# Performance work log

Measured on AMD Instinct MI355X. Metric: run time of the kernel, lower is better.

Reference implementation:

```python
import jax, jax.numpy as jnp
import numpy as np

B, S, H, NH = 4, 1024, 1024, 16
HD = H // NH
I = 4096
EPS = 1e-12
BASE = 10000.0


def setup_inputs() -> dict:
    key = jax.random.key(0)
    ks = jax.random.split(key, 6)
    sc = 0.02
    return {
        "x": jax.random.normal(ks[0], (B, S, H), jnp.float32),
        "ln1_w": jnp.ones((H,), jnp.float32),
        "ln1_b": jnp.zeros((H,), jnp.float32),
        "qkv_w": jax.random.normal(ks[1], (3 * H, H), jnp.float32) * sc,
        "qkv_b": jnp.zeros((3 * H,), jnp.float32),
        "out_w": jax.random.normal(ks[2], (H, H), jnp.float32) * sc,
        "out_b": jnp.zeros((H,), jnp.float32),
        "ln2_w": jnp.ones((H,), jnp.float32),
        "ln2_b": jnp.zeros((H,), jnp.float32),
        "i2h_w": jax.random.normal(ks[3], (2 * I, H), jnp.float32) * sc,
        "i2h_b": jnp.zeros((2 * I,), jnp.float32),
        "h2o_w": jax.random.normal(ks[4], (H, I), jnp.float32) * sc,
        "h2o_b": jnp.zeros((H,), jnp.float32),
    }


def _layer_norm(x, w, b, eps=EPS):
    mu = jnp.mean(x, axis=-1, keepdims=True)
    var = jnp.mean(jnp.square(x - mu), axis=-1, keepdims=True)
    return (x - mu) * jax.lax.rsqrt(var + eps) * w + b


def _rope_cos_sin(seq_len, dim, base):
    # inv_freq = base ** linspace(0, -1 + 2/dim, dim//2), repeated twice
    half = jnp.power(base, jnp.linspace(0.0, -1.0 + 2.0 / dim, dim // 2, dtype=jnp.float32))
    inv_freq = jnp.concatenate([half, half])  # [dim]
    t = jnp.arange(seq_len, dtype=jnp.float32)
    freqs = t[:, None] * inv_freq[None, :]  # [seq, dim]
    return jnp.cos(freqs), jnp.sin(freqs)


def _rotate(x, cos, sin):
    # x: [B, NH, S, HD]; cos/sin: [S, HD]
    xl, xr = jnp.split(x, 2, axis=-1)
    x_rot = jnp.concatenate([-xr, xl], axis=-1)
    return x * cos + x_rot * sin


def _forward(x, ln1_w, ln1_b, qkv_w, qkv_b, out_w, out_b,
             ln2_w, ln2_b, i2h_w, i2h_b, h2o_w, h2o_b):
    b, s, h = x.shape
    # --- LeanSelfAttention (pre-LN, rotary, causal, residual) ---
    h_ln = _layer_norm(x, ln1_w, ln1_b)
    qkv = h_ln @ qkv_w.T + qkv_b  # [b, s, 3h]
    q, k, v = jnp.split(qkv, 3, axis=-1)
    to_heads = lambda t: t.reshape(b, s, NH, HD).transpose(0, 2, 1, 3)  # [b,nh,s,hd]
    q, k, v = to_heads(q), to_heads(k), to_heads(v)
    cos, sin = _rope_cos_sin(s, HD, BASE)
    q, k = _rotate(q, cos, sin), _rotate(k, cos, sin)
    scores = jnp.einsum("bhqd,bhkd->bhqk", q, k) / np.sqrt(HD).astype(np.float32)
    causal = jnp.tril(jnp.ones((s, s), dtype=bool))
    scores = jnp.where(causal, scores, jnp.float32(-10000.0))
    probs = jax.nn.softmax(scores, axis=-1)
    attn = jnp.einsum("bhqk,bhkd->bhqd", probs, v)
    attn = attn.transpose(0, 2, 1, 3).reshape(b, s, h)
    attn_out = attn @ out_w.T + out_b + x  # residual
    # --- LeanFFN (pre-LN, gated gelu, residual) ---
    ffn_ln = _layer_norm(attn_out, ln2_w, ln2_b)
    pre = ffn_ln @ i2h_w.T + i2h_b  # [b, s, 2I]
    gate, lin = jnp.split(pre, 2, axis=-1)
    hid = jax.nn.gelu(gate, approximate=False) * lin
    return hid @ h2o_w.T + h2o_b + attn_out


def reference(x, ln1_w, ln1_b, qkv_w, qkv_b, out_w, out_b,
              ln2_w, ln2_b, i2h_w, i2h_b, h2o_w, h2o_b):
    return _forward(x, ln1_w, ln1_b, qkv_w, qkv_b, out_w, out_b,
                    ln2_w, ln2_b, i2h_w, i2h_b, h2o_w, h2o_b)
```

## Files before the change

### kernel.cpp

```cpp
#include <hip/hip_runtime.h>
#include <cstdint>
#include <cstddef>

typedef __bf16 bf16;
typedef __bf16 bf16x4 __attribute__((ext_vector_type(4)));
typedef __bf16 bf16x8 __attribute__((ext_vector_type(8)));
typedef float  f32x4  __attribute__((ext_vector_type(4)));

#define GLD16(gptr, lptr)                                                      \
  __builtin_amdgcn_global_load_lds(                                            \
      (__attribute__((address_space(1))) unsigned int*)(gptr),                 \
      (__attribute__((address_space(3))) unsigned int*)(lptr), 16, 0, 0)

__global__ __launch_bounds__(256)
void convert_kernel(const float* __restrict__ src, bf16* __restrict__ dst, int n8)
{
    const int j = blockIdx.x * 256 + threadIdx.x;
    if (j >= n8) return;
    const float* s = src + (size_t)j * 8;
    bf16x8 o;
#pragma unroll
    for (int e = 0; e < 8; ++e) o[e] = (bf16)s[e];
    ((bf16x8*)dst)[j] = o;
}

template<class InT>
__global__ __launch_bounds__(256)
void ln_kernel(const InT* __restrict__ x, const float* __restrict__ w,
               const float* __restrict__ b, bf16* __restrict__ out)
{
    __shared__ float red[8];
    const int row = blockIdx.x;
    const int tid = threadIdx.x;
    const InT* xr = x + (size_t)row * 1024;
    float xf[4], s = 0.f, ss = 0.f;
#pragma unroll
    for (int j = 0; j < 4; ++j) {
        xf[j] = (float)xr[tid * 4 + j];
        s += xf[j]; ss += xf[j] * xf[j];
    }
#pragma unroll
    for (int off = 32; off > 0; off >>= 1) { s += __shfl_xor(s, off); ss += __shfl_xor(ss, off); }
    if ((tid & 63) == 0) { red[(tid >> 6) * 2] = s; red[(tid >> 6) * 2 + 1] = ss; }
    __syncthreads();
    s  = red[0] + red[2] + red[4] + red[6];
    ss = red[1] + red[3] + red[5] + red[7];
    const float mu   = s * (1.f / 1024.f);
    const float var  = ss * (1.f / 1024.f) - mu * mu;
    const float rstd = rsqrtf(var + 1e-12f);
    bf16x4 ov;
#pragma unroll
    for (int j = 0; j < 4; ++j)
        ov[j] = (bf16)((xf[j] - mu) * rstd * w[tid * 4 + j] + b[tid * 4 + j]);
    *(bf16x4*)(out + (size_t)row * 1024 + tid * 4) = ov;
}

template<int RES_MODE, bool OUT_F32>
__global__ __launch_bounds__(256)
void gemm_bt(const bf16* __restrict__ A, const bf16* __restrict__ W,
             const float* __restrict__ bias, const void* __restrict__ res,
             void* __restrict__ Cv, int M, int N, int K)
{
    __shared__ alignas(16) bf16 As[128][32];
    __shared__ alignas(16) bf16 Bs[128][32];
    const int tid  = threadIdx.x;
    const int lane = tid & 63, wid = tid >> 6;
    const int lr = lane & 15, lg = lane >> 4;
    const int kgrp = lg * 8;
    const int wm = (wid >> 1) * 64, wn = (wid & 1) * 64;
    const int row0 = blockIdx.x * 128, col0 = blockIdx.y * 128;

    f32x4 acc[4][4] = {};

    for (int k0 = 0; k0 < K; k0 += 32) {
#pragma unroll
        for (int i = 0; i < 2; ++i) {
            const int c = i * 256 + tid;
            const int r = c >> 2, k8 = (c & 3) * 8;
            GLD16(A + (size_t)(row0 + r) * K + k0 + k8,
                  (char*)&As[0][0] + (size_t)(i * 256 + wid * 64) * 16);
            GLD16(W + (size_t)(col0 + r) * K + k0 + k8,
                  (char*)&Bs[0][0] + (size_t)(i * 256 + wid * 64) * 16);
        }
        __syncthreads();
        bf16x8 af[4], bw[4];
#pragma unroll
        for (int mi = 0; mi < 4; ++mi) af[mi] = *(const bf16x8*)&As[wm + mi * 16 + lr][kgrp];
#pragma unroll
        for (int ni = 0; ni < 4; ++ni) bw[ni] = *(const bf16x8*)&Bs[wn + ni * 16 + lr][kgrp];
#pragma unroll
        for (int mi = 0; mi < 4; ++mi)
#pragma unroll
            for (int ni = 0; ni < 4; ++ni)
                acc[mi][ni] = __builtin_amdgcn_mfma_f32_16x16x32_bf16(
                    af[mi], bw[ni], acc[mi][ni], 0, 0, 0);
        __syncthreads();
    }

#pragma unroll
    for (int ni = 0; ni < 4; ++ni) {
        const int ccol = col0 + wn + ni * 16 + lr;
        const float bv = bias[ccol];
#pragma unroll
        for (int mi = 0; mi < 4; ++mi)
#pragma unroll
            for (int r = 0; r < 4; ++r) {
                const size_t crow = (size_t)(row0 + wm + mi * 16 + lg * 4 + r);
                float v = acc[mi][ni][r] + bv;
                if constexpr (RES_MODE == 1) v += ((const float*)res)[crow * N + ccol];
                if constexpr (RES_MODE == 2) v += (float)((const bf16*)res)[crow * N + ccol];
                if constexpr (OUT_F32) ((float*)Cv)[crow * N + ccol] = v;
                else                   ((bf16*)Cv)[crow * N + ccol] = (bf16)v;
            }
    }
}

__global__ __launch_bounds__(256)
void gemm_i2h_gelu(const bf16* __restrict__ A, const bf16* __restrict__ W,
                   const float* __restrict__ bias, bf16* __restrict__ hid)
{
    __shared__ alignas(16) bf16 As[128][32];
    __shared__ alignas(16) bf16 Bg[64][32];
    __shared__ alignas(16) bf16 Bl[64][32];
    const int tid  = threadIdx.x;
    const int lane = tid & 63, wid = tid >> 6;
    const int lr = lane & 15, lg = lane >> 4;
    const int kgrp = lg * 8;
    const int wm = (wid >> 1) * 64, wn = (wid & 1) * 32;
    const int row0 = blockIdx.x * 128, col0 = blockIdx.y * 64;
    const int K = 1024;

    f32x4 accg[4][2] = {}, accl[4][2] = {};

    for (int k0 = 0; k0 < K; k0 += 32) {
#pragma unroll
        for (int i = 0; i < 2; ++i) {
            const int c = i * 256 + tid;
            const int r = c >> 2, k8 = (c & 3) * 8;
            GLD16(A + (size_t)(row0 + r) * K + k0 + k8,
                  (char*)&As[0][0] + (size_t)(i * 256 + wid * 64) * 16);
        }
        {
            const int r = tid >> 2, k8 = (tid & 3) * 8;
            GLD16(W + (size_t)(col0 + r) * K + k0 + k8,
                  (char*)&Bg[0][0] + (size_t)(wid * 64) * 16);
            GLD16(W + (size_t)(4096 + col0 + r) * K + k0 + k8,
                  (char*)&Bl[0][0] + (size_t)(wid * 64) * 16);
        }
        __syncthreads();
        bf16x8 af[4], bg[2], bl[2];
#pragma unroll
        for (int mi = 0; mi < 4; ++mi) af[mi] = *(const bf16x8*)&As[wm + mi * 16 + lr][kgrp];
#pragma unroll
        for (int ni = 0; ni < 2; ++ni) {
            bg[ni] = *(const bf16x8*)&Bg[wn + ni * 16 + lr][kgrp];
            bl[ni] = *(const bf16x8*)&Bl[wn + ni * 16 + lr][kgrp];
        }
#pragma unroll
        for (int mi = 0; mi < 4; ++mi)
#pragma unroll
            for (int ni = 0; ni < 2; ++ni) {
                accg[mi][ni] = __builtin_amdgcn_mfma_f32_16x16x32_bf16(
                    af[mi], bg[ni], accg[mi][ni], 0, 0, 0);
                accl[mi][ni] = __builtin_amdgcn_mfma_f32_16x16x32_bf16(
                    af[mi], bl[ni], accl[mi][ni], 0, 0, 0);
            }
        __syncthreads();
    }

#pragma unroll
    for (int ni = 0; ni < 2; ++ni) {
        const int gc = col0 + wn + ni * 16 + lr;
        const float bg_ = bias[gc], bl_ = bias[4096 + gc];
#pragma unroll
        for (int mi = 0; mi < 4; ++mi)
#pragma unroll
            for (int r = 0; r < 4; ++r) {
                const size_t crow = (size_t)(row0 + wm + mi * 16 + lg * 4 + r);
                const float g = accg[mi][ni][r] + bg_;
                const float l = accl[mi][ni][r] + bl_;
                const float ge = 0.5f * g * (1.f + erff(g * 0.70710678118654752f));
                hid[crow * 4096 + gc] = (bf16)(ge * l);
            }
    }
}

__global__ __launch_bounds__(256)
void rope_kernel(const bf16* __restrict__ qkv, bf16* __restrict__ q_r,
                 bf16* __restrict__ k_r, bf16* __restrict__ v_r)
{
    const int g  = blockIdx.x * 256 + threadIdx.x;
    const int i  = g & 31;
    const int h  = (g >> 5) & 15;
    const int bs = g >> 9;
    const int s  = bs & 1023;
    const bf16* base = qkv + (size_t)bs * 3072;
    const float inv = __expf((float)i * (-9.210340371976184f / 32.f));
    const float ang = (float)s * inv;
    float sn, c;
    sincosf(ang, &sn, &c);
    const int qoff = h * 64 + i;
    const float ql = (float)base[qoff],        qh = (float)base[qoff + 32];
    const float kl = (float)base[1024 + qoff], kh = (float)base[1024 + qoff + 32];
    const size_t ob = ((size_t)((bs >> 10) * 16 + h) * 1024 + s) * 64;
    q_r[ob + i]      = (bf16)(ql * c - qh * sn);
    q_r[ob + i + 32] = (bf16)(qh * c + ql * sn);
    k_r[ob + i]      = (bf16)(kl * c - kh * sn);
    k_r[ob + i + 32] = (bf16)(kh * c + kl * sn);
    v_r[ob + i]      = base[2048 + qoff];
    v_r[ob + i + 32] = base[2048 + qoff + 32];
}

__global__ __launch_bounds__(256)
void attn_kernel(const bf16* __restrict__ q_r, const bf16* __restrict__ k_r,
                 const bf16* __restrict__ v_r, bf16* __restrict__ attn)
{
    __shared__ alignas(16) bf16 Ks[64][72];
    __shared__ alignas(16) bf16 Vt[64][72];
    __shared__ alignas(16) bf16 Ps[4][16][72];
    const int qt = blockIdx.x, bh = blockIdx.y;
    const int tid = threadIdx.x, lane = tid & 63, w = tid >> 6;
    const int lr = lane & 15, lg = lane >> 4;
    const int kgrp = lg * 8;
    const int qbase = qt * 64;

    const bf16* qrow = q_r + ((size_t)bh * 1024 + qbase + w * 16 + lr) * 64;
    const bf16x8 qf0 = *(const bf16x8*)(qrow + kgrp);
    const bf16x8 qf1 = *(const bf16x8*)(qrow + 32 + kgrp);

    f32x4 o[4] = {};
    float m_r[4], l_r[4];
#pragma unroll
    for (int r = 0; r < 4; ++r) { m_r[r] = -1e30f; l_r[r] = 0.f; }

    const int nchunk = qt + 1;
    for (int ic = 0; ic < nchunk; ++ic) {
        const int kb = ic * 64;
        __syncthreads();
#pragma unroll
        for (int i = 0; i < 2; ++i) {
            const int c = i * 256 + tid;
            const int row = c >> 3, e8 = (c & 7) * 8;
            *(bf16x8*)&Ks[row][e8] =
                *(const bf16x8*)(k_r + ((size_t)bh * 1024 + kb + row) * 64 + e8);
            const bf16x8 vv =
                *(const bf16x8*)(v_r + ((size_t)bh * 1024 + kb + row) * 64 + e8);
#pragma unroll
            for (int j = 0; j < 8; ++j) Vt[e8 + j][row] = vv[j];
        }
        __syncthreads();

        f32x4 sv[4] = {};
#pragma unroll
        for (int nb = 0; nb < 4; ++nb) {
            const bf16x8 kf0 = *(const bf16x8*)&Ks[nb * 16 + lr][kgrp];
            const bf16x8 kf1 = *(const bf16x8*)&Ks[nb * 16 + lr][32 + kgrp];
            sv[nb] = __builtin_amdgcn_mfma_f32_16x16x32_bf16(qf0, kf0, sv[nb], 0, 0, 0);
            sv[nb] = __builtin_amdgcn_mfma_f32_16x16x32_bf16(qf1, kf1, sv[nb], 0, 0, 0);
        }

        const bool diag = (kb == qbase);
        float pv[4][4];
#pragma unroll
        for (int r = 0; r < 4; ++r) {
            float s0[4];
#pragma unroll
            for (int nb = 0; nb < 4; ++nb) {
                float t = sv[nb][r] * 0.125f;
                if (diag && (nb * 16 + lr) > (w * 16 + lg * 4 + r)) t = -10000.f;
                s0[nb] = t;
            }
            float rm = fmaxf(fmaxf(s0[0], s0[1]), fmaxf(s0[2], s0[3]));
#pragma unroll
            for (int off = 1; off < 16; off <<= 1) rm = fmaxf(rm, __shfl_xor(rm, off));
            const float nm = fmaxf(m_r[r], rm);
            const float sc = __expf(m_r[r] - nm);
            float rs = 0.f;
#pragma unroll
            for (int nb = 0; nb < 4; ++nb) {
                const float p = __expf(s0[nb] - nm);
                pv[nb][r] = p; rs += p;
            }
#pragma unroll
            for (int off = 1; off < 16; off <<= 1) rs += __shfl_xor(rs, off);
            l_r[r] = l_r[r] * sc + rs;
            m_r[r] = nm;
#pragma unroll
            for (int nb = 0; nb < 4; ++nb) o[nb][r] *= sc;
        }

#pragma unroll
        for (int nb = 0; nb < 4; ++nb)
#pragma unroll
            for (int r = 0; r < 4; ++r)
                Ps[w][lg * 4 + r][nb * 16 + lr] = (bf16)pv[nb][r];
#pragma unroll
        for (int nb = 0; nb < 4; ++nb)
#pragma unroll
            for (int ks = 0; ks < 2; ++ks) {
                const bf16x8 pa = *(const bf16x8*)&Ps[w][lr][ks * 32 + kgrp];
                const bf16x8 vb = *(const bf16x8*)&Vt[nb * 16 + lr][ks * 32 + kgrp];
                o[nb] = __builtin_amdgcn_mfma_f32_16x16x32_bf16(pa, vb, o[nb], 0, 0, 0);
            }
    }

    const int b = bh >> 4, head = bh & 15;
#pragma unroll
    for (int nb = 0; nb < 4; ++nb)
#pragma unroll
        for (int r = 0; r < 4; ++r) {
            const size_t rw = (size_t)(b * 1024 + qbase + w * 16 + lg * 4 + r);
            attn[rw * 1024 + head * 64 + nb * 16 + lr] = (bf16)(o[nb][r] / l_r[r]);
        }
}

extern "C" void kernel_launch(void* const* d_in, const int* in_sizes, int n_in,
                              void* d_out, int out_size, void* d_ws, size_t ws_size,
                              hipStream_t stream)
{
    const float* x    = (const float*)d_in[0];
    const float* ln1w = (const float*)d_in[1];
    const float* ln1b = (const float*)d_in[2];
    const float* qkvw = (const float*)d_in[3];
    const float* qkvb = (const float*)d_in[4];
    const float* outw = (const float*)d_in[5];
    const float* outb = (const float*)d_in[6];
    const float* ln2w = (const float*)d_in[7];
    const float* ln2b = (const float*)d_in[8];
    const float* i2hw = (const float*)d_in[9];
    const float* i2hb = (const float*)d_in[10];
    const float* h2ow = (const float*)d_in[11];
    const float* h2ob = (const float*)d_in[12];

    char* ws = (char*)d_ws;
    const size_t MB = 1024 * 1024;

    bf16* h_ln    = (bf16*)(ws + 0);
    bf16* qkv     = (bf16*)(ws + 8 * MB);
    bf16* q_r     = (bf16*)(ws + 32 * MB);
    bf16* k_r     = (bf16*)(ws + 40 * MB);
    bf16* v_r     = (bf16*)(ws + 48 * MB);
    bf16* attn    = (bf16*)(ws + 56 * MB);
    bf16* attnout = (bf16*)(ws + 64 * MB);
    bf16* ffnln   = (bf16*)(ws + 72 * MB);
    bf16* hid     = (bf16*)(ws + 80 * MB);
    bf16* qkvw_c  = (bf16*)(ws + 112 * MB);
    bf16* outw_c  = (bf16*)(ws + 118 * MB);
    bf16* i2hw_c  = (bf16*)(ws + 120 * MB);
    bf16* h2ow_c  = (bf16*)(ws + 136 * MB);

    convert_kernel<<<1536, 256, 0, stream>>>(qkvw, qkvw_c, 3145728 / 8);
    convert_kernel<<< 512, 256, 0, stream>>>(outw, outw_c, 1048576 / 8);
    convert_kernel<<<4096, 256, 0, stream>>>(i2hw, i2hw_c, 8388608 / 8);
    convert_kernel<<<2048, 256, 0, stream>>>(h2ow, h2ow_c, 4194304 / 8);

    ln_kernel<float><<<4096, 256, 0, stream>>>(x, ln1w, ln1b, h_ln);
    gemm_bt<0, false><<<dim3(32, 24), 256, 0, stream>>>(
        h_ln, qkvw_c, qkvb, nullptr, qkv, 4096, 3072, 1024);
    rope_kernel<<<8192, 256, 0, stream>>>(qkv, q_r, k_r, v_r);
    attn_kernel<<<dim3(16, 64), 256, 0, stream>>>(q_r, k_r, v_r, attn);
    gemm_bt<1, false><<<dim3(32, 8), 256, 0, stream>>>(
        attn, outw_c, outb, x, attnout, 4096, 1024, 1024);
    ln_kernel<bf16><<<4096, 256, 0, stream>>>(attnout, ln2w, ln2b, ffnln);
    gemm_i2h_gelu<<<dim3(32, 64), 256, 0, stream>>>(ffnln, i2hw_c, i2hb, hid);
    gemm_bt<2, true><<<dim3(32, 8), 256, 0, stream>>>(
        hid, h2ow_c, h2ob, attnout, d_out, 4096, 1024, 4096);
}
```

Before: 484.7 us.

## Fuse RoPE into QKV GEMM epilogue and pipeline i2h GEMM with triple-buffered LDS

The standalone rope kernel is removed: the QKV projection writes rotated Q/K and head-major V directly from its GEMM epilogue, pairing columns i and i+32 inside each 64-column warp tile. This drops the intermediate qkv buffer round trip and one launch. Separately, the gated i2h GEMM is rewritten with 512-thread blocks, 256x128 tiles, triple-buffered async global-to-LDS loads with XOR swizzling, and setprio around the MFMA bursts, to raise data reuse and overlap loads with compute. Risks include higher register pressure and less occupancy in the larger kernel, and the epilogue recomputing sincos per element.

```diff
diff --git a/kernel.cpp b/kernel.cpp
--- a/kernel.cpp
+++ b/kernel.cpp
@@ -116,21 +116,21 @@
 }
 
 __global__ __launch_bounds__(256)
-void gemm_i2h_gelu(const bf16* __restrict__ A, const bf16* __restrict__ W,
-                   const float* __restrict__ bias, bf16* __restrict__ hid)
+void gemm_qkv_rope(const bf16* __restrict__ A, const bf16* __restrict__ W,
+                   const float* __restrict__ bias, bf16* __restrict__ q_r,
+                   bf16* __restrict__ k_r, bf16* __restrict__ v_r)
 {
     __shared__ alignas(16) bf16 As[128][32];
-    __shared__ alignas(16) bf16 Bg[64][32];
-    __shared__ alignas(16) bf16 Bl[64][32];
+    __shared__ alignas(16) bf16 Bs[128][32];
     const int tid  = threadIdx.x;
     const int lane = tid & 63, wid = tid >> 6;
     const int lr = lane & 15, lg = lane >> 4;
     const int kgrp = lg * 8;
-    const int wm = (wid >> 1) * 64, wn = (wid & 1) * 32;
-    const int row0 = blockIdx.x * 128, col0 = blockIdx.y * 64;
+    const int wm = (wid >> 1) * 64, wn = (wid & 1) * 64;
+    const int row0 = blockIdx.x * 128, col0 = blockIdx.y * 128;
     const int K = 1024;
 
-    f32x4 accg[4][2] = {}, accl[4][2] = {};
+    f32x4 acc[4][4] = {};
 
     for (int k0 = 0; k0 < K; k0 += 32) {
 #pragma unroll
@@ -139,76 +139,162 @@
             const int r = c >> 2, k8 = (c & 3) * 8;
             GLD16(A + (size_t)(row0 + r) * K + k0 + k8,
                   (char*)&As[0][0] + (size_t)(i * 256 + wid * 64) * 16);
-        }
-        {
-            const int r = tid >> 2, k8 = (tid & 3) * 8;
             GLD16(W + (size_t)(col0 + r) * K + k0 + k8,
-                  (char*)&Bg[0][0] + (size_t)(wid * 64) * 16);
-            GLD16(W + (size_t)(4096 + col0 + r) * K + k0 + k8,
-                  (char*)&Bl[0][0] + (size_t)(wid * 64) * 16);
-        }
-        __syncthreads();
-        bf16x8 af[4], bg[2], bl[2];
+                  (char*)&Bs[0][0] + (size_t)(i * 256 + wid * 64) * 16);
+        }
+        __syncthreads();
+        bf16x8 af[4], bw[4];
 #pragma unroll
         for (int mi = 0; mi < 4; ++mi) af[mi] = *(const bf16x8*)&As[wm + mi * 16 + lr][kgrp];
 #pragma unroll
-        for (int ni = 0; ni < 2; ++ni) {
-            bg[ni] = *(const bf16x8*)&Bg[wn + ni * 16 + lr][kgrp];
-            bl[ni] = *(const bf16x8*)&Bl[wn + ni * 16 + lr][kgrp];
-        }
-#pragma unroll
-        for (int mi = 0; mi < 4; ++mi)
-#pragma unroll
-            for (int ni = 0; ni < 2; ++ni) {
-                accg[mi][ni] = __builtin_amdgcn_mfma_f32_16x16x32_bf16(
-                    af[mi], bg[ni], accg[mi][ni], 0, 0, 0);
-                accl[mi][ni] = __builtin_amdgcn_mfma_f32_16x16x32_bf16(
-                    af[mi], bl[ni], accl[mi][ni], 0, 0, 0);
-            }
-        __syncthreads();
-    }
-
+        for (int ni = 0; ni < 4; ++ni) bw[ni] = *(const bf16x8*)&Bs[wn + ni * 16 + lr][kgrp];
+#pragma unroll
+        for (int mi = 0; mi < 4; ++mi)
+#pragma unroll
+            for (int ni = 0; ni < 4; ++ni)
+                acc[mi][ni] = __builtin_amdgcn_mfma_f32_16x16x32_bf16(
+                    af[mi], bw[ni], acc[mi][ni], 0, 0, 0);
+        __syncthreads();
+    }
+
+    const int third = blockIdx.y >> 3;
+    bf16* dst = (third == 0) ? q_r : (third == 1) ? k_r : v_r;
 #pragma unroll
     for (int ni = 0; ni < 2; ++ni) {
-        const int gc = col0 + wn + ni * 16 + lr;
-        const float bg_ = bias[gc], bl_ = bias[4096 + gc];
+        const int i_ = ni * 16 + lr;
+        const int ccol = col0 + wn + ni * 16 + lr;
+        const int h = (ccol >> 6) & 15;
+        const float blo = bias[ccol], bhi = bias[ccol + 32];
+        const float inv = __expf((float)i_ * (-9.210340371976184f / 32.f));
 #pragma unroll
         for (int mi = 0; mi < 4; ++mi)
 #pragma unroll
             for (int r = 0; r < 4; ++r) {
-                const size_t crow = (size_t)(row0 + wm + mi * 16 + lg * 4 + r);
-                const float g = accg[mi][ni][r] + bg_;
-                const float l = accl[mi][ni][r] + bl_;
+                const int crow = row0 + wm + mi * 16 + lg * 4 + r;
+                const int s = crow & 1023, b = crow >> 10;
+                const float lo = acc[mi][ni][r] + blo;
+                const float hi = acc[mi][ni + 2][r] + bhi;
+                const size_t ob = ((size_t)(b * 16 + h) * 1024 + s) * 64;
+                if (third == 2) {
+                    dst[ob + i_]      = (bf16)lo;
+                    dst[ob + i_ + 32] = (bf16)hi;
+                } else {
+                    float sn, c;
+                    sincosf((float)s * inv, &sn, &c);
+                    dst[ob + i_]      = (bf16)(lo * c - hi * sn);
+                    dst[ob + i_ + 32] = (bf16)(hi * c + lo * sn);
+                }
+            }
+    }
+}
+
+__global__ __launch_bounds__(512, 2)
+void gemm_i2h_g8(const bf16* __restrict__ A, const bf16* __restrict__ W,
+                 const float* __restrict__ bias, bf16* __restrict__ hid)
+{
+    __shared__ alignas(16) char smem[3 * 32768];
+    const int tid  = threadIdx.x;
+    const int lane = tid & 63, wid = tid >> 6;
+    const int lrr  = lane & 15, lg = lane >> 4;
+    const int wr = wid >> 2, wc = wid & 3;
+    const int row0 = blockIdx.x * 256;
+    const int colh = blockIdx.y * 128 + wc * 32;
+    const int NT = 32;
+
+    const int cA0 = tid, cA1 = 512 + tid;
+    const int rA0 = cA0 >> 2, rA1 = cA1 >> 2, rB = tid >> 2;
+    const int swA0 = (((cA0 & 3) * 16) ^ (((rA0 >> 1) & 3) << 4)) >> 1;
+    const int swA1 = (((cA1 & 3) * 16) ^ (((rA1 >> 1) & 3) << 4)) >> 1;
+    const int swB  = (((tid & 3) * 16) ^ (((rB  >> 1) & 3) << 4)) >> 1;
+    const bf16* gA0 = A + (size_t)(row0 + rA0) * 1024 + swA0;
+    const bf16* gA1 = A + (size_t)(row0 + rA1) * 1024 + swA1;
+    const bf16* gBg = W + (size_t)(blockIdx.y * 128 + rB) * 1024 + swB;
+    const bf16* gBl = W + (size_t)(4096 + blockIdx.y * 128 + rB) * 1024 + swB;
+    const int dA0 = (wid * 64) * 16, dA1 = (512 + wid * 64) * 16, dB = (wid * 64) * 16;
+
+    f32x4 acc[8][4] = {};
+
+    {
+        char* b0 = smem;
+        GLD16(gBg, b0 + 16384 + dB); GLD16(gBl, b0 + 24576 + dB);
+        GLD16(gA0, b0 + dA0);        GLD16(gA1, b0 + dA1);
+        char* b1 = smem + 32768;
+        GLD16(gBg + 32, b1 + 16384 + dB); GLD16(gBl + 32, b1 + 24576 + dB);
+        GLD16(gA0 + 32, b1 + dA0);        GLD16(gA1 + 32, b1 + dA1);
+    }
+    asm volatile("s_waitcnt vmcnt(4)\ns_barrier" ::: "memory");
+
+    int cur = 0, stg = 2;
+    for (int t = 0; t < NT; ++t) {
+        const char* bA  = smem + cur * 32768;
+        const char* bBg = bA + 16384;
+        const char* bBl = bA + 24576;
+        char* sB = smem + stg * 32768;
+        const int k0s = (t + 2) * 32;
+        const bool dostg = (t < NT - 2);
+
+        if (dostg) { GLD16(gBg + k0s, sB + 16384 + dB); GLD16(gBl + k0s, sB + 24576 + dB); }
+        bf16x8 bf[4], af[4];
+        const int bcol = lg * 16;
+#pragma unroll
+        for (int nv = 0; nv < 4; ++nv) {
+            const int row = wc * 32 + (nv & 1) * 16 + lrr;
+            const char* base = (nv < 2) ? bBg : bBl;
+            bf[nv] = *(const bf16x8*)(base + row * 64 + (bcol ^ (((row >> 1) & 3) << 4)));
+        }
+#pragma unroll
+        for (int mi = 0; mi < 4; ++mi) {
+            const int row = wr * 128 + mi * 16 + lrr;
+            af[mi] = *(const bf16x8*)(bA + row * 64 + (bcol ^ (((row >> 1) & 3) << 4)));
+        }
+        __builtin_amdgcn_s_barrier();
+        __builtin_amdgcn_s_setprio(1);
+#pragma unroll
+        for (int mi = 0; mi < 4; ++mi)
+#pragma unroll
+            for (int nv = 0; nv < 4; ++nv)
+                acc[mi][nv] = __builtin_amdgcn_mfma_f32_16x16x32_bf16(
+                    af[mi], bf[nv], acc[mi][nv], 0, 0, 0);
+        __builtin_amdgcn_s_setprio(0);
+        __builtin_amdgcn_s_barrier();
+
+        if (dostg) { GLD16(gA0 + k0s, sB + dA0); GLD16(gA1 + k0s, sB + dA1); }
+#pragma unroll
+        for (int mi = 0; mi < 4; ++mi) {
+            const int row = wr * 128 + (4 + mi) * 16 + lrr;
+            af[mi] = *(const bf16x8*)(bA + row * 64 + (bcol ^ (((row >> 1) & 3) << 4)));
+        }
+        __builtin_amdgcn_s_barrier();
+        __builtin_amdgcn_s_setprio(1);
+#pragma unroll
+        for (int mi = 0; mi < 4; ++mi)
+#pragma unroll
+            for (int nv = 0; nv < 4; ++nv)
+                acc[4 + mi][nv] = __builtin_amdgcn_mfma_f32_16x16x32_bf16(
+                    af[mi], bf[nv], acc[4 + mi][nv], 0, 0, 0);
+        __builtin_amdgcn_s_setprio(0);
+
+        if (dostg) asm volatile("s_waitcnt vmcnt(4)\ns_barrier" ::: "memory");
+        else       asm volatile("s_waitcnt vmcnt(0)\ns_barrier" ::: "memory");
+        cur = (cur == 2) ? 0 : cur + 1;
+        stg = (stg == 2) ? 0 : stg + 1;
+    }
+
+#pragma unroll
+    for (int c = 0; c < 2; ++c) {
+        const int gcol = colh + c * 16 + lrr;
+        const float bg_ = bias[gcol], bl_ = bias[4096 + gcol];
+#pragma unroll
+        for (int mi = 0; mi < 8; ++mi)
+#pragma unroll
+            for (int r = 0; r < 4; ++r) {
+                const size_t row = (size_t)(row0 + wr * 128 + mi * 16 + lg * 4 + r);
+                const float g = acc[mi][c][r] + bg_;
+                const float l = acc[mi][2 + c][r] + bl_;
                 const float ge = 0.5f * g * (1.f + erff(g * 0.70710678118654752f));
-                hid[crow * 4096 + gc] = (bf16)(ge * l);
-            }
-    }
-}
-
-__global__ __launch_bounds__(256)
-void rope_kernel(const bf16* __restrict__ qkv, bf16* __restrict__ q_r,
-                 bf16* __restrict__ k_r, bf16* __restrict__ v_r)
-{
-    const int g  = blockIdx.x * 256 + threadIdx.x;
-    const int i  = g & 31;
-    const int h  = (g >> 5) & 15;
-    const int bs = g >> 9;
-    const int s  = bs & 1023;
-    const bf16* base = qkv + (size_t)bs * 3072;
-    const float inv = __expf((float)i * (-9.210340371976184f / 32.f));
-    const float ang = (float)s * inv;
-    float sn, c;
-    sincosf(ang, &sn, &c);
-    const int qoff = h * 64 + i;
-    const float ql = (float)base[qoff],        qh = (float)base[qoff + 32];
-    const float kl = (float)base[1024 + qoff], kh = (float)base[1024 + qoff + 32];
-    const size_t ob = ((size_t)((bs >> 10) * 16 + h) * 1024 + s) * 64;
-    q_r[ob + i]      = (bf16)(ql * c - qh * sn);
-    q_r[ob + i + 32] = (bf16)(qh * c + ql * sn);
-    k_r[ob + i]      = (bf16)(kl * c - kh * sn);
-    k_r[ob + i + 32] = (bf16)(kh * c + kl * sn);
-    v_r[ob + i]      = base[2048 + qoff];
-    v_r[ob + i + 32] = base[2048 + qoff + 32];
+                hid[row * 4096 + gcol] = (bf16)(ge * l);
+            }
+    }
 }
 
 __global__ __launch_bounds__(256)
@@ -336,18 +422,17 @@
     const size_t MB = 1024 * 1024;
 
     bf16* h_ln    = (bf16*)(ws + 0);
-    bf16* qkv     = (bf16*)(ws + 8 * MB);
-    bf16* q_r     = (bf16*)(ws + 32 * MB);
-    bf16* k_r     = (bf16*)(ws + 40 * MB);
-    bf16* v_r     = (bf16*)(ws + 48 * MB);
-    bf16* attn    = (bf16*)(ws + 56 * MB);
-    bf16* attnout = (bf16*)(ws + 64 * MB);
-    bf16* ffnln   = (bf16*)(ws + 72 * MB);
-    bf16* hid     = (bf16*)(ws + 80 * MB);
-    bf16* qkvw_c  = (bf16*)(ws + 112 * MB);
-    bf16* outw_c  = (bf16*)(ws + 118 * MB);
-    bf16* i2hw_c  = (bf16*)(ws + 120 * MB);
-    bf16* h2ow_c  = (bf16*)(ws + 136 * MB);
+    bf16* q_r     = (bf16*)(ws + 8 * MB);
+    bf16* k_r     = (bf16*)(ws + 16 * MB);
+    bf16* v_r     = (bf16*)(ws + 24 * MB);
+    bf16* attn    = (bf16*)(ws + 32 * MB);
+    bf16* attnout = (bf16*)(ws + 40 * MB);
+    bf16* ffnln   = (bf16*)(ws + 48 * MB);
+    bf16* hid     = (bf16*)(ws + 56 * MB);
+    bf16* qkvw_c  = (bf16*)(ws + 88 * MB);
+    bf16* outw_c  = (bf16*)(ws + 94 * MB);
+    bf16* i2hw_c  = (bf16*)(ws + 96 * MB);
+    bf16* h2ow_c  = (bf16*)(ws + 112 * MB);
 
     convert_kernel<<<1536, 256, 0, stream>>>(qkvw, qkvw_c, 3145728 / 8);
     convert_kernel<<< 512, 256, 0, stream>>>(outw, outw_c, 1048576 / 8);
@@ -355,14 +440,13 @@
     convert_kernel<<<2048, 256, 0, stream>>>(h2ow, h2ow_c, 4194304 / 8);
 
     ln_kernel<float><<<4096, 256, 0, stream>>>(x, ln1w, ln1b, h_ln);
-    gemm_bt<0, false><<<dim3(32, 24), 256, 0, stream>>>(
-        h_ln, qkvw_c, qkvb, nullptr, qkv, 4096, 3072, 1024);
-    rope_kernel<<<8192, 256, 0, stream>>>(qkv, q_r, k_r, v_r);
+    gemm_qkv_rope<<<dim3(32, 24), 256, 0, stream>>>(h_ln, qkvw_c, qkvb,
+                                                    q_r, k_r, v_r);
     attn_kernel<<<dim3(16, 64), 256, 0, stream>>>(q_r, k_r, v_r, attn);
     gemm_bt<1, false><<<dim3(32, 8), 256, 0, stream>>>(
         attn, outw_c, outb, x, attnout, 4096, 1024, 1024);
     ln_kernel<bf16><<<4096, 256, 0, stream>>>(attnout, ln2w, ln2b, ffnln);
-    gemm_i2h_gelu<<<dim3(32, 64), 256, 0, stream>>>(ffnln, i2hw_c, i2hb, hid);
+    gemm_i2h_g8<<<dim3(16, 32), 512, 0, stream>>>(ffnln, i2hw_c, i2hb, hid);
     gemm_bt<2, true><<<dim3(32, 8), 256, 0, stream>>>(
         hid, h2ow_c, h2ob, attnout, d_out, 4096, 1024, 4096);
 }
```

Measured after the change: 484.9 us. No clear change (+0.0%).
